# Performance work log

Hardware: AMD Instinct MI355X
Metric: run time of the kernel (lower is better)

## Reference

```python
import jax, jax.numpy as jnp
import numpy as np

RANK = 64
N_GAMMA = 7   # g{r}0..g{r}6 scalars per component
N_ALPHA = 64  # a{r}0..a{r}63 scalars per component


def setup_inputs() -> dict:
    key = jax.random.key(0)
    x = jax.random.normal(key, (131072, N_GAMMA, N_ALPHA), dtype=jnp.float32)
    # All scalar parameters are initialized to 0.2 in the original module.
    beta_0 = jnp.array(0.2, dtype=jnp.float32)
    gamma = jnp.full((RANK, N_GAMMA), 0.2, dtype=jnp.float32)  # g{r}{i}
    alpha = jnp.full((RANK, N_ALPHA), 0.2, dtype=jnp.float32)  # a{r}{j}
    return {"x": x, "beta_0": beta_0, "gamma": gamma, "alpha": alpha}


def reference(x, beta_0, gamma, alpha):
    # W = sum_r gamma_r (outer) alpha_r ; y_n = beta_0 + <W, X_n>
    w = jnp.einsum("ri,rj->ij", gamma, alpha)       # [7, 64]
    y = beta_0 + jnp.einsum("nij,ij->n", x, w)      # [N]
    return y
```

## Files before the change

kernel.cpp:

```cpp
#include <hip/hip_runtime.h>

#define RANK    64
#define N_GAMMA 7
#define N_ALPHA 64
#define WLEN    (N_GAMMA * N_ALPHA)

__global__ void __launch_bounds__(512) compute_w_kernel(
    const float* __restrict__ gamma,
    const float* __restrict__ alpha,
    float* __restrict__ w) {
    int t = threadIdx.x;
    if (t < WLEN) {
        int i = t >> 6;
        int j = t & 63;
        float s = 0.f;
#pragma unroll
        for (int r = 0; r < RANK; ++r)
            s = fmaf(gamma[r * N_GAMMA + i], alpha[r * N_ALPHA + j], s);
        w[t] = s;
    }
}

__global__ void __launch_bounds__(256) cp_dot_kernel(
    const float4* __restrict__ x4,
    const float* __restrict__ beta,
    const float* __restrict__ w,
    float* __restrict__ y,
    int nGroups) {
    const int lane = threadIdx.x & 63;
    const float4* __restrict__ w4 = (const float4*)w;

    float4 wv[7];
    int rowid[7];
#pragma unroll
    for (int i = 0; i < 7; ++i) {
        int j = i * 64 + lane;
        rowid[i] = j / 112;
        wv[i] = w4[j % 112];
    }
    const float beta0 = beta[0];

    const int wave   = blockIdx.x * (blockDim.x >> 6) + (threadIdx.x >> 6);
    const int nWaves = gridDim.x * (blockDim.x >> 6);

    for (int g = wave; g < nGroups; g += nWaves) {
        const float4* __restrict__ p = x4 + (size_t)g * 448;
        float a0 = 0.f, a1 = 0.f, a2 = 0.f, a3 = 0.f;
#pragma unroll
        for (int i = 0; i < 7; ++i) {
            float4 v = p[i * 64 + lane];
            float dot = fmaf(v.x, wv[i].x,
                        fmaf(v.y, wv[i].y,
                        fmaf(v.z, wv[i].z, v.w * wv[i].w)));
            a0 += (rowid[i] == 0) ? dot : 0.f;
            a1 += (rowid[i] == 1) ? dot : 0.f;
            a2 += (rowid[i] == 2) ? dot : 0.f;
            a3 += (rowid[i] == 3) ? dot : 0.f;
        }
#pragma unroll
        for (int off = 32; off >= 1; off >>= 1) {
            a0 += __shfl_xor(a0, off, 64);
            a1 += __shfl_xor(a1, off, 64);
            a2 += __shfl_xor(a2, off, 64);
            a3 += __shfl_xor(a3, off, 64);
        }
        if (lane < 4) {
            float v = (lane == 0) ? a0 : (lane == 1) ? a1 : (lane == 2) ? a2 : a3;
            y[g * 4 + lane] = beta0 + v;
        }
    }
}

extern "C" void kernel_launch(void* const* d_in, const int* in_sizes, int n_in,
                              void* d_out, int out_size, void* d_ws, size_t ws_size,
                              hipStream_t stream) {
    const float* x     = (const float*)d_in[0];
    const float* beta  = (const float*)d_in[1];
    const float* gamma = (const float*)d_in[2];
    const float* alpha = (const float*)d_in[3];
    float* y = (float*)d_out;
    float* w = (float*)d_ws;

    const int n = in_sizes[0] / WLEN;
    const int nGroups = n / 4;

    compute_w_kernel<<<1, 512, 0, stream>>>(gamma, alpha, w);

    const int blocks = 2048;
    cp_dot_kernel<<<blocks, 256, 0, stream>>>((const float4*)x, beta, w, y, nGroups);
}
```

Before: 320.2 us.

## Fuse weight computation into dot kernel and use transpose-style shuffle reduction

Removes the separate single-block kernel that builds W. Each block now recomputes W into shared memory and then loads its per-lane float4 weights from there, which saves a launch and its serialization at the cost of redundant per-block work. The per-group reduction is also restructured: row-boundary predicates combine the partial dot products into four accumulators, and a butterfly reduction merges them across lanes so far fewer shuffles are needed than four full 6-step reductions. All loads of x are issued up front.

Measured after the change: 322.3 us. No clear change (+0.6%).

```diff
diff --git a/kernel.cpp b/kernel.cpp
--- a/kernel.cpp
+++ b/kernel.cpp
@@ -5,68 +5,84 @@
 #define N_ALPHA 64
 #define WLEN    (N_GAMMA * N_ALPHA)
 
-__global__ void __launch_bounds__(512) compute_w_kernel(
+__device__ __forceinline__ float dot4(const float4 a, const float4 b) {
+    return fmaf(a.x, b.x, fmaf(a.y, b.y, fmaf(a.z, b.z, a.w * b.w)));
+}
+
+__global__ void __launch_bounds__(256) cp_fused_kernel(
+    const float4* __restrict__ x4,
+    const float* __restrict__ beta,
     const float* __restrict__ gamma,
     const float* __restrict__ alpha,
-    float* __restrict__ w) {
-    int t = threadIdx.x;
-    if (t < WLEN) {
+    float* __restrict__ y,
+    int nGroups) {
+    __shared__ float w_lds[WLEN];
+
+    for (int t = threadIdx.x; t < WLEN; t += blockDim.x) {
         int i = t >> 6;
         int j = t & 63;
         float s = 0.f;
 #pragma unroll
         for (int r = 0; r < RANK; ++r)
             s = fmaf(gamma[r * N_GAMMA + i], alpha[r * N_ALPHA + j], s);
-        w[t] = s;
+        w_lds[t] = s;
     }
-}
+    __syncthreads();
 
-__global__ void __launch_bounds__(256) cp_dot_kernel(
-    const float4* __restrict__ x4,
-    const float* __restrict__ beta,
-    const float* __restrict__ w,
-    float* __restrict__ y,
-    int nGroups) {
     const int lane = threadIdx.x & 63;
-    const float4* __restrict__ w4 = (const float4*)w;
 
     float4 wv[7];
-    int rowid[7];
 #pragma unroll
     for (int i = 0; i < 7; ++i) {
         int j = i * 64 + lane;
-        rowid[i] = j / 112;
-        wv[i] = w4[j % 112];
+        wv[i] = *(const float4*)&w_lds[4 * (j % 112)];
     }
     const float beta0 = beta[0];
+
+    const bool p1 = lane < 48;
+    const bool p3 = lane < 32;
+    const bool p5 = lane < 16;
 
     const int wave   = blockIdx.x * (blockDim.x >> 6) + (threadIdx.x >> 6);
     const int nWaves = gridDim.x * (blockDim.x >> 6);
 
     for (int g = wave; g < nGroups; g += nWaves) {
         const float4* __restrict__ p = x4 + (size_t)g * 448;
-        float a0 = 0.f, a1 = 0.f, a2 = 0.f, a3 = 0.f;
-#pragma unroll
-        for (int i = 0; i < 7; ++i) {
-            float4 v = p[i * 64 + lane];
-            float dot = fmaf(v.x, wv[i].x,
-                        fmaf(v.y, wv[i].y,
-                        fmaf(v.z, wv[i].z, v.w * wv[i].w)));
-            a0 += (rowid[i] == 0) ? dot : 0.f;
-            a1 += (rowid[i] == 1) ? dot : 0.f;
-            a2 += (rowid[i] == 2) ? dot : 0.f;
-            a3 += (rowid[i] == 3) ? dot : 0.f;
-        }
-#pragma unroll
-        for (int off = 32; off >= 1; off >>= 1) {
-            a0 += __shfl_xor(a0, off, 64);
-            a1 += __shfl_xor(a1, off, 64);
-            a2 += __shfl_xor(a2, off, 64);
-            a3 += __shfl_xor(a3, off, 64);
-        }
-        if (lane < 4) {
-            float v = (lane == 0) ? a0 : (lane == 1) ? a1 : (lane == 2) ? a2 : a3;
-            y[g * 4 + lane] = beta0 + v;
+        float4 v0 = p[0 * 64 + lane];
+        float4 v1 = p[1 * 64 + lane];
+        float4 v2 = p[2 * 64 + lane];
+        float4 v3 = p[3 * 64 + lane];
+        float4 v4 = p[4 * 64 + lane];
+        float4 v5 = p[5 * 64 + lane];
+        float4 v6 = p[6 * 64 + lane];
+        float d0 = dot4(v0, wv[0]);
+        float d1 = dot4(v1, wv[1]);
+        float d2 = dot4(v2, wv[2]);
+        float d3 = dot4(v3, wv[3]);
+        float d4 = dot4(v4, wv[4]);
+        float d5 = dot4(v5, wv[5]);
+        float d6 = dot4(v6, wv[6]);
+        float a0 = d0 + (p1 ? d1 : 0.f);
+        float a1 = d2 + (p1 ? 0.f : d1) + (p3 ? d3 : 0.f);
+        float a2 = d4 + (p3 ? 0.f : d3) + (p5 ? d5 : 0.f);
+        float a3 = d6 + (p5 ? 0.f : d5);
+
+        float c0 = a0 + __shfl_xor(a0, 32, 64);
+        float c1 = a1 + __shfl_xor(a1, 32, 64);
+        float c2 = a2 + __shfl_xor(a2, 32, 64);
+        float c3 = a3 + __shfl_xor(a3, 32, 64);
+        float d01 = (lane & 32) ? c1 : c0;
+        float d23 = (lane & 32) ? c3 : c2;
+        d01 += __shfl_xor(d01, 16, 64);
+        d23 += __shfl_xor(d23, 16, 64);
+        float f = (lane & 16) ? d23 : d01;
+        f += __shfl_xor(f, 8, 64);
+        f += __shfl_xor(f, 4, 64);
+        f += __shfl_xor(f, 2, 64);
+        f += __shfl_xor(f, 1, 64);
+        if ((lane & 15) == 0) {
+            int r = ((lane >> 4) & 1) * 2 + ((lane >> 5) & 1);
+            y[g * 4 + r] = beta0 + f;
         }
     }
 }
@@ -79,13 +95,10 @@
     const float* gamma = (const float*)d_in[2];
     const float* alpha = (const float*)d_in[3];
     float* y = (float*)d_out;
-    float* w = (float*)d_ws;
 
     const int n = in_sizes[0] / WLEN;
     const int nGroups = n / 4;
 
-    compute_w_kernel<<<1, 512, 0, stream>>>(gamma, alpha, w);
-
     const int blocks = 2048;
-    cp_dot_kernel<<<blocks, 256, 0, stream>>>((const float4*)x, beta, w, y, nGroups);
+    cp_fused_kernel<<<blocks, 256, 0, stream>>>((const float4*)x, beta, gamma, alpha, y, nGroups);
 }
```
